# Performance work log

Measured on AMD Instinct MI355X. Metric: run time of the kernel, lower is better.

The kernel has to match this reference:

```python
import jax, jax.numpy as jnp
import numpy as np

N, F, F_, H = 8192, 512, 64, 8
NEG = -1e10

def setup_inputs() -> dict:
    key = jax.random.key(0)
    k1, k2, k3, k4 = jax.random.split(key, 4)
    X = jax.random.normal(k1, (N, F), dtype=jnp.float32)
    A = jax.random.randint(k2, (N, N), 0, 2).astype(jnp.float32)  # dense 0/1 adjacency
    kernels = jax.random.normal(k3, (H, F, F_), dtype=jnp.float32) * 0.05
    attn_kernels = jax.random.normal(k4, (H, 2 * F_), dtype=jnp.float32) * 0.05
    return {"X": X, "A": A, "kernels": kernels, "attn_kernels": attn_kernels}

def reference(X, A, kernels, attn_kernels):
    # Per-head linear transform: [H, N, F_]
    WX = jnp.einsum('nf,hfo->hno', X, kernels)
    a1 = attn_kernels[:, :F_]   # [H, F_] acts on source (row) node
    a2 = attn_kernels[:, F_:]   # [H, F_] acts on target (col) node
    # score[h,i,j] = a1_h . WX[h,i] + a2_h . WX[h,j]  (outer sum, no N^2*2F_ tensor)
    s1 = jnp.einsum('hno,ho->hn', WX, a1)  # [H, N]
    s2 = jnp.einsum('hno,ho->hn', WX, a2)  # [H, N]
    scores = s1[:, :, None] + s2[:, None, :]  # [H, N, N]
    # adjacency mask: A==0 -> -1e10 (note: original has no LeakyReLU)
    masked = jnp.where(A[None, :, :] == 0.0, scores + NEG, scores)
    attn = jax.nn.softmax(masked, axis=-1)  # [H, N, N]
    # dropout is identity at inference (Keras Dropout without training=True)
    feats = jnp.einsum('hnm,hmo->hno', attn, WX)  # [H, N, F_]
    feats = jax.nn.relu(feats)  # concat reduction applies activation per head
    out = jnp.transpose(feats, (1, 0, 2)).reshape(N, H * F_)  # concat heads
    return out
```

## Files before the change

kernel.cpp:

```cpp
#include <hip/hip_runtime.h>
#include <cstdint>

#define NN 8192
#define FF 512
#define FO 64
#define NH 8
#define LDYE 520
#define YPART (8192 * 520)
#define SPLITK 3


typedef __attribute__((ext_vector_type(8))) __bf16 bf16x8;
typedef __attribute__((ext_vector_type(4))) float f32x4;

__device__ __forceinline__ unsigned short f2bf(float f) {
    unsigned int u = __float_as_uint(f);
    u += 0x7fffu + ((u >> 16) & 1u);
    return (unsigned short)(u >> 16);
}

__device__ __forceinline__ void gload16(const void* g, void* l) {
    __builtin_amdgcn_global_load_lds(
        (const __attribute__((address_space(1))) unsigned int*)g,
        (__attribute__((address_space(3))) unsigned int*)l,
        16, 0, 0);
}

__global__ __launch_bounds__(256) void k_convA8(const float* __restrict__ A,
                                                unsigned char* __restrict__ Ab) {
    const int b = blockIdx.x, t = threadIdx.x;
    const int rt = b >> 8;
    const int k16 = ((b & 255) << 1) | (t & 1);
    const int row = t >> 1;
    const uint4* src = (const uint4*)(A + (((size_t)(rt * 128 + row)) << 13) + k16 * 16);
    uint4 f0 = src[0], f1 = src[1], f2 = src[2], f3 = src[3];
#define PK8(v) (((v.x >> 22) & 0x38u) | (((v.y >> 22) & 0x38u) << 8) | \
                (((v.z >> 22) & 0x38u) << 16) | (((v.w >> 22) & 0x38u) << 24))
    uint4 o = {PK8(f0), PK8(f1), PK8(f2), PK8(f3)};
#undef PK8
    size_t G = (((size_t)(rt * 512 + k16)) << 7) + row;
    *(uint4*)(Ab + (G << 4)) = o;
}

__global__ __launch_bounds__(256) void k_prep(const float* __restrict__ X,
                                              const float* __restrict__ Kw,
                                              unsigned short* __restrict__ Xb,
                                              unsigned short* __restrict__ Ktb) {
    const int b = blockIdx.x;
    const int t = threadIdx.x;
    if (b < 2048) {
        size_t base = ((size_t)b * 256 + t) * 8;
        float4 a = *(const float4*)(X + base);
        float4 c = *(const float4*)(X + base + 4);
        ushort4 o0, o1;
        o0.x = f2bf(a.x); o0.y = f2bf(a.y); o0.z = f2bf(a.z); o0.w = f2bf(a.w);
        o1.x = f2bf(c.x); o1.y = f2bf(c.y); o1.z = f2bf(c.z); o1.w = f2bf(c.w);
        *(ushort4*)(Xb + base) = o0;
        *(ushort4*)(Xb + base + 4) = o1;
    } else {
        int h = b - 2048;
        for (int e = t; e < FF * FO; e += 256) {
            int o = e >> 9, f = e & 511;
            Ktb[(size_t)h * FF * FO + e] = f2bf(Kw[(size_t)h * FF * FO + (size_t)f * FO + o]);
        }
    }
}

union WxSmem {
    struct { unsigned short Xs[4096]; unsigned short Ks[2048]; } s;
    unsigned char Vs[64][144];
};

__global__ __launch_bounds__(256) void k_wx(const unsigned short* __restrict__ Xb,
                                            const unsigned short* __restrict__ Ktb,
                                            const float* __restrict__ Aw,
                                            unsigned char* __restrict__ Vt) {
    __shared__ WxSmem sm;
    const int t = threadIdx.x;
    const int n0 = blockIdx.x * 128;
    const int h = blockIdx.y;
    const int lane = t & 63, w = t >> 6;
    const int quad = lane >> 4, l15 = lane & 15;

    const unsigned short* xS0 = Xb + (size_t)(n0 + (t & 127)) * FF + (t >> 7) * 8;
    const unsigned short* xS1 = Xb + (size_t)(n0 + ((t + 256) & 127)) * FF + ((t + 256) >> 7) * 8;
    unsigned short* xD0 = sm.s.Xs + t * 8;
    unsigned short* xD1 = sm.s.Xs + (t + 256) * 8;
    const unsigned short* kS = Ktb + (size_t)h * FF * FO + (size_t)(t & 63) * FF + (t >> 6) * 8;
    unsigned short* kD = sm.s.Ks + t * 8;

    const bf16x8* aF[2];
    const bf16x8* bF[4];
    for (int i = 0; i < 2; ++i)
        aF[i] = (const bf16x8*)(sm.s.Xs + (size_t)(quad * 128 + w * 32 + i * 16 + l15) * 8);
    for (int j = 0; j < 4; ++j)
        bF[j] = (const bf16x8*)(sm.s.Ks + (size_t)(quad * 64 + j * 16 + l15) * 8);

    f32x4 acc[2][4] = {};
    for (int f0 = 0; f0 < FF; f0 += 32) {
        gload16(xS0 + f0, xD0);
        gload16(xS1 + f0, xD1);
        gload16(kS + f0, kD);
        __syncthreads();
        bf16x8 av[2], bv[4];
        for (int i = 0; i < 2; ++i) av[i] = aF[i][0];
        for (int j = 0; j < 4; ++j) bv[j] = bF[j][0];
        for (int i = 0; i < 2; ++i)
            for (int j = 0; j < 4; ++j)
                acc[i][j] = __builtin_amdgcn_mfma_f32_16x16x32_bf16(av[i], bv[j], acc[i][j], 0, 0, 0);
        __syncthreads();
    }

    float a2v[4];
    for (int j = 0; j < 4; ++j) a2v[j] = Aw[h * 128 + 64 + j * 16 + l15];
    float ex[2][4];
    for (int i = 0; i < 2; ++i)
        for (int r = 0; r < 4; ++r) {
            float p = acc[i][0][r] * a2v[0] + acc[i][1][r] * a2v[1]
                    + acc[i][2][r] * a2v[2] + acc[i][3][r] * a2v[3];
            p += __shfl_xor(p, 1);
            p += __shfl_xor(p, 2);
            p += __shfl_xor(p, 4);
            p += __shfl_xor(p, 8);
            ex[i][r] = __expf(p);
        }

    for (int i = 0; i < 2; ++i)
        for (int j = 0; j < 4; ++j) {
            int rowb = w * 32 + i * 16 + quad * 4;
            int col = j * 16 + l15;
            unsigned u = __builtin_amdgcn_cvt_pk_fp8_f32(
                ex[i][0] * acc[i][j][0], ex[i][1] * acc[i][j][1], 0, false);
            u = __builtin_amdgcn_cvt_pk_fp8_f32(
                ex[i][2] * acc[i][j][2], ex[i][3] * acc[i][j][3], (int)u, true);
            *(unsigned*)&sm.Vs[col][rowb] = u;
        }
    __syncthreads();
    for (int j2 = 0; j2 < 2; ++j2) {
        int vid = t + j2 * 256;
        int o = vid >> 3, k16o = vid & 7;
        size_t H = (size_t)((n0 >> 4) + k16o) * 640 + h * 64 + o;
        *(uint4*)(Vt + (H << 4)) = *(const uint4*)&sm.Vs[o][k16o * 16];
    }
    if (l15 == 0) {
        for (int i = 0; i < 2; ++i)
            for (int r = 0; r < 4; ++r) {
                int row = w * 32 + i * 16 + quad * 4 + r;
                unsigned u = __builtin_amdgcn_cvt_pk_fp8_f32(ex[i][r], ex[i][r], 0, false);
                size_t H = (size_t)((n0 >> 4) + (row >> 4)) * 640 + 512 + h;
                Vt[(H << 4) + (row & 15)] = (unsigned char)(u & 0xff);
            }
    }
}

__global__ __launch_bounds__(256) void k_gemm(const unsigned char* __restrict__ Ab,
                                              const unsigned char* __restrict__ Vt,
                                              float* __restrict__ Y) {
    __shared__ unsigned char As[8192];
    __shared__ unsigned char Bs[10240];
    const int t = threadIdx.x;
    const int id = blockIdx.x;
    const int xcd = id & 7;
    const int u = id >> 3;
    const int ct = u & 3;
    const int rp = ((u >> 2) << 3) | xcd;
    const int rt = rp & 63;
    const int part = rp >> 6;
    const int ks0 = (part * 128) / SPLITK;
    const int ks1 = ((part + 1) * 128) / SPLITK;

    const unsigned char* aS0 = Ab + ((size_t)rt << 20) + (size_t)t * 16;
    const unsigned char* aS1 = aS0 + 4096;
    unsigned char* aD0 = As + t * 16;
    unsigned char* aD1 = aD0 + 4096;
    const int g1 = t + 256, g2 = t + 512;
    const unsigned char* bS0 = Vt + (size_t)((t / 160) * 10240 + (ct * 160 + t % 160) * 16);
    const unsigned char* bS1 = Vt + (size_t)((g1 / 160) * 10240 + (ct * 160 + g1 % 160) * 16);
    const unsigned char* bS2 = Vt + (size_t)((g2 / 160) * 10240 + (ct * 160 + g2 % 160) * 16);
    unsigned char* bD0 = Bs + t * 16;
    unsigned char* bD1 = Bs + g1 * 16;
    unsigned char* bD2 = Bs + g2 * 16;

    const int lane = t & 63;
    const int w = t >> 6;
    const int wm = w >> 1, wn = w & 1;
    const int quad = lane >> 4, l15 = lane & 15;

    int aOff[4], bOff[5];
    for (int i = 0; i < 4; ++i)
        aOff[i] = (quad >> 1) * 2048 + (quad & 1) * 8 + (wm * 64 + i * 16 + l15) * 16;
    for (int j = 0; j < 5; ++j)
        bOff[j] = (quad >> 1) * 2560 + (quad & 1) * 8 + (wn * 80 + j * 16 + l15) * 16;

    f32x4 acc[4][5] = {};

    for (int ks = ks0; ks < ks1; ++ks) {
        const size_t koA = (size_t)ks << 13;
        const size_t koB = (size_t)ks * 40960;
        gload16(aS0 + koA, aD0);
        gload16(aS1 + koA, aD1);
        gload16(bS0 + koB, bD0);
        gload16(bS1 + koB, bD1);
        if (t < 128) gload16(bS2 + koB, bD2);
        __syncthreads();
#pragma unroll
        for (int h2 = 0; h2 < 2; ++h2) {
            long long av[4], bv[5];
            for (int i = 0; i < 4; ++i)
                av[i] = *(const long long*)(As + aOff[i] + h2 * 4096);
            for (int j = 0; j < 5; ++j)
                bv[j] = *(const long long*)(Bs + bOff[j] + h2 * 5120);
            for (int i = 0; i < 4; ++i)
                for (int j = 0; j < 5; ++j)
                    acc[i][j] = __builtin_amdgcn_mfma_f32_16x16x32_fp8_fp8(av[i], bv[j], acc[i][j], 0, 0, 0);
        }
        __syncthreads();
    }

    float* Yp = Y + (size_t)part * YPART;
    for (int i = 0; i < 4; ++i) {
        int row = rt * 128 + wm * 64 + i * 16 + quad * 4;
        for (int j = 0; j < 5; ++j) {
            int col = ct * 160 + wn * 80 + j * 16 + l15;
            if (col < 520) {
                for (int r = 0; r < 4; ++r)
                    Yp[(size_t)(row + r) * LDYE + col] = acc[i][j][r];
            }
        }
    }
}

__global__ __launch_bounds__(256) void k_epi(const float* __restrict__ Y,
                                             float* __restrict__ out) {
    int idx = blockIdx.x * 256 + threadIdx.x;
    int n = idx >> 7;
    int c = (idx & 127) * 4;
    int h = c >> 6;
    float4 u = {0.f, 0.f, 0.f, 0.f};
    float den = 0.f;
    const float* yp = Y + (size_t)n * LDYE;
#pragma unroll
    for (int p = 0; p < SPLITK; ++p) {
        float4 v = *(const float4*)(yp + c);
        u.x += v.x; u.y += v.y; u.z += v.z; u.w += v.w;
        den += yp[512 + h];
        yp += (size_t)YPART;
    }
    float inv = 1.0f / den;
    float4 o;
    o.x = fmaxf(u.x * inv, 0.f);
    o.y = fmaxf(u.y * inv, 0.f);
    o.z = fmaxf(u.z * inv, 0.f);
    o.w = fmaxf(u.w * inv, 0.f);
    *(float4*)(out + (size_t)n * 512 + c) = o;
}

extern "C" void kernel_launch(void* const* d_in, const int* in_sizes, int n_in,
                              void* d_out, int out_size, void* d_ws, size_t ws_size,
                              hipStream_t stream) {
    const float* X  = (const float*)d_in[0];
    const float* A  = (const float*)d_in[1];
    const float* Kw = (const float*)d_in[2];
    const float* Aw = (const float*)d_in[3];
    float* out = (float*)d_out;
    char* ws = (char*)d_ws;
    unsigned char* Ab = (unsigned char*)ws;
    unsigned char* Vt = (unsigned char*)(ws + (size_t)67108864);
    float* Yb = (float*)(ws + (size_t)67108864 + (size_t)5242880);
    unsigned short* Xb = (unsigned short*)Yb;
    unsigned short* Ktb = Xb + (size_t)NN * FF;

    k_convA8<<<dim3(16384), dim3(256), 0, stream>>>(A, Ab);
    k_prep<<<dim3(2056), dim3(256), 0, stream>>>(X, Kw, Xb, Ktb);
    k_wx<<<dim3(64, 8), dim3(256), 0, stream>>>(Xb, Ktb, Aw, Vt);
    k_gemm<<<dim3(768), dim3(256), 0, stream>>>(Ab, Vt, Yb);
    k_epi<<<dim3(4096), dim3(256), 0, stream>>>(Yb, out);
}
```

Before: 511.9 us.

## Double-buffer LDS tiles in fp8 GEMM and linearize A conversion stores

The GEMM main loop now uses two LDS buffers, so the global-to-LDS loads for the next k-step are issued before the MFMA work on the current tile, with one barrier per iteration instead of two. This is meant to hide global load latency behind matrix math. It doubles LDS use per block, which may reduce occupancy. The A-to-fp8 conversion kernel is also reindexed so each thread writes consecutive 16-byte chunks, making the stores fully linear, though the reads become strided across rows.

```diff
diff --git a/kernel.cpp b/kernel.cpp
--- a/kernel.cpp
+++ b/kernel.cpp
@@ -28,18 +28,17 @@
 
 __global__ __launch_bounds__(256) void k_convA8(const float* __restrict__ A,
                                                 unsigned char* __restrict__ Ab) {
-    const int b = blockIdx.x, t = threadIdx.x;
-    const int rt = b >> 8;
-    const int k16 = ((b & 255) << 1) | (t & 1);
-    const int row = t >> 1;
-    const uint4* src = (const uint4*)(A + (((size_t)(rt * 128 + row)) << 13) + k16 * 16);
+    const size_t gid = (size_t)blockIdx.x * 256 + threadIdx.x;
+    const int row127 = (int)(gid & 127);
+    const int k16 = (int)((gid >> 7) & 511);
+    const int rt = (int)(gid >> 16);
+    const uint4* src = (const uint4*)(A + (((size_t)(rt * 128 + row127)) << 13) + k16 * 16);
     uint4 f0 = src[0], f1 = src[1], f2 = src[2], f3 = src[3];
 #define PK8(v) (((v.x >> 22) & 0x38u) | (((v.y >> 22) & 0x38u) << 8) | \
                 (((v.z >> 22) & 0x38u) << 16) | (((v.w >> 22) & 0x38u) << 24))
     uint4 o = {PK8(f0), PK8(f1), PK8(f2), PK8(f3)};
 #undef PK8
-    size_t G = (((size_t)(rt * 512 + k16)) << 7) + row;
-    *(uint4*)(Ab + (G << 4)) = o;
+    *(uint4*)(Ab + (gid << 4)) = o;
 }
 
 __global__ __launch_bounds__(256) void k_prep(const float* __restrict__ X,
@@ -156,8 +155,8 @@
 __global__ __launch_bounds__(256) void k_gemm(const unsigned char* __restrict__ Ab,
                                               const unsigned char* __restrict__ Vt,
                                               float* __restrict__ Y) {
-    __shared__ unsigned char As[8192];
-    __shared__ unsigned char Bs[10240];
+    __shared__ unsigned char As0[8192], As1[8192];
+    __shared__ unsigned char Bs0[10240], Bs1[10240];
     const int t = threadIdx.x;
     const int id = blockIdx.x;
     const int xcd = id & 7;
@@ -171,15 +170,10 @@
 
     const unsigned char* aS0 = Ab + ((size_t)rt << 20) + (size_t)t * 16;
     const unsigned char* aS1 = aS0 + 4096;
-    unsigned char* aD0 = As + t * 16;
-    unsigned char* aD1 = aD0 + 4096;
     const int g1 = t + 256, g2 = t + 512;
     const unsigned char* bS0 = Vt + (size_t)((t / 160) * 10240 + (ct * 160 + t % 160) * 16);
     const unsigned char* bS1 = Vt + (size_t)((g1 / 160) * 10240 + (ct * 160 + g1 % 160) * 16);
     const unsigned char* bS2 = Vt + (size_t)((g2 / 160) * 10240 + (ct * 160 + g2 % 160) * 16);
-    unsigned char* bD0 = Bs + t * 16;
-    unsigned char* bD1 = Bs + g1 * 16;
-    unsigned char* bD2 = Bs + g2 * 16;
 
     const int lane = t & 63;
     const int w = t >> 6;
@@ -194,28 +188,49 @@
 
     f32x4 acc[4][5] = {};
 
+#define STAGE(ks, AD, BD)                                                      \
+    do {                                                                       \
+        const size_t koA = (size_t)(ks) << 13;                                 \
+        const size_t koB = (size_t)(ks) * 40960;                               \
+        gload16(aS0 + koA, (AD) + t * 16);                                     \
+        gload16(aS1 + koA, (AD) + 4096 + t * 16);                              \
+        gload16(bS0 + koB, (BD) + t * 16);                                     \
+        gload16(bS1 + koB, (BD) + g1 * 16);                                    \
+        if (t < 128) gload16(bS2 + koB, (BD) + g2 * 16);                       \
+    } while (0)
+
+#define MFMA_TILE(AS, BS)                                                      \
+    do {                                                                       \
+        _Pragma("unroll")                                                      \
+        for (int h2 = 0; h2 < 2; ++h2) {                                       \
+            long long av[4], bv[5];                                            \
+            for (int i = 0; i < 4; ++i)                                        \
+                av[i] = *(const long long*)((AS) + aOff[i] + h2 * 4096);       \
+            for (int j = 0; j < 5; ++j)                                        \
+                bv[j] = *(const long long*)((BS) + bOff[j] + h2 * 5120);       \
+            for (int i = 0; i < 4; ++i)                                        \
+                for (int j = 0; j < 5; ++j)                                    \
+                    acc[i][j] = __builtin_amdgcn_mfma_f32_16x16x32_fp8_fp8(    \
+                        av[i], bv[j], acc[i][j], 0, 0, 0);                     \
+        }                                                                      \
+    } while (0)
+
+    STAGE(ks0, As0, Bs0);
+    __syncthreads();
+    int p = 0;
     for (int ks = ks0; ks < ks1; ++ks) {
-        const size_t koA = (size_t)ks << 13;
-        const size_t koB = (size_t)ks * 40960;
-        gload16(aS0 + koA, aD0);
-        gload16(aS1 + koA, aD1);
-        gload16(bS0 + koB, bD0);
-        gload16(bS1 + koB, bD1);
-        if (t < 128) gload16(bS2 + koB, bD2);
+        if (p == 0) {
+            if (ks + 1 < ks1) STAGE(ks + 1, As1, Bs1);
+            MFMA_TILE(As0, Bs0);
+        } else {
+            if (ks + 1 < ks1) STAGE(ks + 1, As0, Bs0);
+            MFMA_TILE(As1, Bs1);
+        }
         __syncthreads();
-#pragma unroll
-        for (int h2 = 0; h2 < 2; ++h2) {
-            long long av[4], bv[5];
-            for (int i = 0; i < 4; ++i)
-                av[i] = *(const long long*)(As + aOff[i] + h2 * 4096);
-            for (int j = 0; j < 5; ++j)
-                bv[j] = *(const long long*)(Bs + bOff[j] + h2 * 5120);
-            for (int i = 0; i < 4; ++i)
-                for (int j = 0; j < 5; ++j)
-                    acc[i][j] = __builtin_amdgcn_mfma_f32_16x16x32_fp8_fp8(av[i], bv[j], acc[i][j], 0, 0, 0);
-        }
-        __syncthreads();
-    }
+        p ^= 1;
+    }
+#undef STAGE
+#undef MFMA_TILE
 
     float* Yp = Y + (size_t)part * YPART;
     for (int i = 0; i < 4; ++i) {
```

Result: slower. 561.7 us (+9.7%).

## Load GEMM fragments directly from global memory with register double-buffering

Applied to the files above, without the earlier changes.

Changes the fp8 layouts of the adjacency matrix and the V matrix so each lane's MFMA operand is 16 contiguous bytes in global memory. The GEMM then drops its LDS staging and barriers, and instead prefetches the next k-step's fragments into registers while computing the current one. The conversion and WX kernels write the new interleaved layout, with the exponent column staged through shared memory. This removes LDS traffic and block-level synchronisation, but each wave now loads operands from global or L2 with no sharing across waves, which raises global traffic and register pressure.

```diff
diff --git a/kernel.cpp b/kernel.cpp
--- a/kernel.cpp
+++ b/kernel.cpp
@@ -12,6 +12,7 @@
 
 typedef __attribute__((ext_vector_type(8))) __bf16 bf16x8;
 typedef __attribute__((ext_vector_type(4))) float f32x4;
+typedef __attribute__((ext_vector_type(2))) long long llx2;
 
 __device__ __forceinline__ unsigned short f2bf(float f) {
     unsigned int u = __float_as_uint(f);
@@ -28,18 +29,22 @@
 
 __global__ __launch_bounds__(256) void k_convA8(const float* __restrict__ A,
                                                 unsigned char* __restrict__ Ab) {
-    const int b = blockIdx.x, t = threadIdx.x;
-    const int rt = b >> 8;
-    const int k16 = ((b & 255) << 1) | (t & 1);
-    const int row = t >> 1;
-    const uint4* src = (const uint4*)(A + (((size_t)(rt * 128 + row)) << 13) + k16 * 16);
-    uint4 f0 = src[0], f1 = src[1], f2 = src[2], f3 = src[3];
+    const size_t gid = (size_t)blockIdx.x * 256 + threadIdx.x;
+    const int row = (int)(gid & 127);
+    const int q   = (int)((gid >> 7) & 3);
+    const int ks  = (int)((gid >> 9) & 127);
+    const int rt  = (int)(gid >> 16);
+    const float* src = A + (((size_t)(rt * 128 + row)) << 13) + ks * 64 + q * 8;
+    float4 f0 = *(const float4*)(src);
+    float4 f1 = *(const float4*)(src + 4);
+    float4 f2 = *(const float4*)(src + 32);
+    float4 f3 = *(const float4*)(src + 36);
 #define PK8(v) (((v.x >> 22) & 0x38u) | (((v.y >> 22) & 0x38u) << 8) | \
                 (((v.z >> 22) & 0x38u) << 16) | (((v.w >> 22) & 0x38u) << 24))
-    uint4 o = {PK8(f0), PK8(f1), PK8(f2), PK8(f3)};
+    uint4 fi0 = *(uint4*)&f0, fi1 = *(uint4*)&f1, fi2 = *(uint4*)&f2, fi3 = *(uint4*)&f3;
+    uint4 o = {PK8(fi0), PK8(fi1), PK8(fi2), PK8(fi3)};
 #undef PK8
-    size_t G = (((size_t)(rt * 512 + k16)) << 7) + row;
-    *(uint4*)(Ab + (G << 4)) = o;
+    *(uint4*)(Ab + (gid << 4)) = o;
 }
 
 __global__ __launch_bounds__(256) void k_prep(const float* __restrict__ X,
@@ -68,7 +73,7 @@
 
 union WxSmem {
     struct { unsigned short Xs[4096]; unsigned short Ks[2048]; } s;
-    unsigned char Vs[64][144];
+    struct { unsigned char Vs[64][144]; unsigned char Es[128]; } r;
 };
 
 __global__ __launch_bounds__(256) void k_wx(const unsigned short* __restrict__ Xb,
@@ -133,31 +138,38 @@
                 ex[i][0] * acc[i][j][0], ex[i][1] * acc[i][j][1], 0, false);
             u = __builtin_amdgcn_cvt_pk_fp8_f32(
                 ex[i][2] * acc[i][j][2], ex[i][3] * acc[i][j][3], (int)u, true);
-            *(unsigned*)&sm.Vs[col][rowb] = u;
-        }
-    __syncthreads();
-    for (int j2 = 0; j2 < 2; ++j2) {
-        int vid = t + j2 * 256;
-        int o = vid >> 3, k16o = vid & 7;
-        size_t H = (size_t)((n0 >> 4) + k16o) * 640 + h * 64 + o;
-        *(uint4*)(Vt + (H << 4)) = *(const uint4*)&sm.Vs[o][k16o * 16];
-    }
+            *(unsigned*)&sm.r.Vs[col][rowb] = u;
+        }
     if (l15 == 0) {
         for (int i = 0; i < 2; ++i)
             for (int r = 0; r < 4; ++r) {
                 int row = w * 32 + i * 16 + quad * 4 + r;
                 unsigned u = __builtin_amdgcn_cvt_pk_fp8_f32(ex[i][r], ex[i][r], 0, false);
-                size_t H = (size_t)((n0 >> 4) + (row >> 4)) * 640 + 512 + h;
-                Vt[(H << 4) + (row & 15)] = (unsigned char)(u & 0xff);
+                sm.r.Es[row] = (unsigned char)(u & 0xff);
             }
+    }
+    __syncthreads();
+    for (int j2 = 0; j2 < 2; ++j2) {
+        int vid = t + j2 * 256;
+        int o = vid & 63, q = (vid >> 6) & 3, ksl = vid >> 8;
+        const unsigned char* src = &sm.r.Vs[o][ksl * 64 + q * 8];
+        uint2 lo = *(const uint2*)src;
+        uint2 hi = *(const uint2*)(src + 32);
+        uint4 g = {lo.x, lo.y, hi.x, hi.y};
+        *(uint4*)(Vt + (size_t)((n0 >> 6) + ksl) * 40960 + q * 10240 + (h * 64 + o) * 16) = g;
+    }
+    if (t < 8) {
+        int ksl = t >> 2, q = t & 3;
+        uint2 lo = *(const uint2*)&sm.r.Es[ksl * 64 + q * 8];
+        uint2 hi = *(const uint2*)&sm.r.Es[ksl * 64 + 32 + q * 8];
+        uint4 g = {lo.x, lo.y, hi.x, hi.y};
+        *(uint4*)(Vt + (size_t)((n0 >> 6) + ksl) * 40960 + q * 10240 + (512 + h) * 16) = g;
     }
 }
 
 __global__ __launch_bounds__(256) void k_gemm(const unsigned char* __restrict__ Ab,
                                               const unsigned char* __restrict__ Vt,
                                               float* __restrict__ Y) {
-    __shared__ unsigned char As[8192];
-    __shared__ unsigned char Bs[10240];
     const int t = threadIdx.x;
     const int id = blockIdx.x;
     const int xcd = id & 7;
@@ -169,52 +181,40 @@
     const int ks0 = (part * 128) / SPLITK;
     const int ks1 = ((part + 1) * 128) / SPLITK;
 
-    const unsigned char* aS0 = Ab + ((size_t)rt << 20) + (size_t)t * 16;
-    const unsigned char* aS1 = aS0 + 4096;
-    unsigned char* aD0 = As + t * 16;
-    unsigned char* aD1 = aD0 + 4096;
-    const int g1 = t + 256, g2 = t + 512;
-    const unsigned char* bS0 = Vt + (size_t)((t / 160) * 10240 + (ct * 160 + t % 160) * 16);
-    const unsigned char* bS1 = Vt + (size_t)((g1 / 160) * 10240 + (ct * 160 + g1 % 160) * 16);
-    const unsigned char* bS2 = Vt + (size_t)((g2 / 160) * 10240 + (ct * 160 + g2 % 160) * 16);
-    unsigned char* bD0 = Bs + t * 16;
-    unsigned char* bD1 = Bs + g1 * 16;
-    unsigned char* bD2 = Bs + g2 * 16;
-
     const int lane = t & 63;
     const int w = t >> 6;
     const int wm = w >> 1, wn = w & 1;
     const int quad = lane >> 4, l15 = lane & 15;
 
-    int aOff[4], bOff[5];
-    for (int i = 0; i < 4; ++i)
-        aOff[i] = (quad >> 1) * 2048 + (quad & 1) * 8 + (wm * 64 + i * 16 + l15) * 16;
-    for (int j = 0; j < 5; ++j)
-        bOff[j] = (quad >> 1) * 2560 + (quad & 1) * 8 + (wn * 80 + j * 16 + l15) * 16;
+    const unsigned char* aP = Ab + ((size_t)rt << 20) + quad * 2048 + (wm * 64 + l15) * 16;
+    const unsigned char* bP = Vt + quad * 10240 + (ct * 160 + wn * 80 + l15) * 16;
 
     f32x4 acc[4][5] = {};
+    llx2 a_cur[4], b_cur[5];
+    {
+        const unsigned char* ap = aP + (size_t)ks0 * 8192;
+        const unsigned char* bp = bP + (size_t)ks0 * 40960;
+        for (int i = 0; i < 4; ++i) a_cur[i] = *(const llx2*)(ap + i * 256);
+        for (int j = 0; j < 5; ++j) b_cur[j] = *(const llx2*)(bp + j * 256);
+    }
 
     for (int ks = ks0; ks < ks1; ++ks) {
-        const size_t koA = (size_t)ks << 13;
-        const size_t koB = (size_t)ks * 40960;
-        gload16(aS0 + koA, aD0);
-        gload16(aS1 + koA, aD1);
-        gload16(bS0 + koB, bD0);
-        gload16(bS1 + koB, bD1);
-        if (t < 128) gload16(bS2 + koB, bD2);
-        __syncthreads();
-#pragma unroll
-        for (int h2 = 0; h2 < 2; ++h2) {
-            long long av[4], bv[5];
-            for (int i = 0; i < 4; ++i)
-                av[i] = *(const long long*)(As + aOff[i] + h2 * 4096);
+        const int ksn = (ks + 1 < ks1) ? ks + 1 : ks;
+        const unsigned char* ap = aP + (size_t)ksn * 8192;
+        const unsigned char* bp = bP + (size_t)ksn * 40960;
+        llx2 a_nxt[4], b_nxt[5];
+        for (int i = 0; i < 4; ++i) a_nxt[i] = *(const llx2*)(ap + i * 256);
+        for (int j = 0; j < 5; ++j) b_nxt[j] = *(const llx2*)(bp + j * 256);
+        for (int i = 0; i < 4; ++i)
             for (int j = 0; j < 5; ++j)
-                bv[j] = *(const long long*)(Bs + bOff[j] + h2 * 5120);
-            for (int i = 0; i < 4; ++i)
-                for (int j = 0; j < 5; ++j)
-                    acc[i][j] = __builtin_amdgcn_mfma_f32_16x16x32_fp8_fp8(av[i], bv[j], acc[i][j], 0, 0, 0);
-        }
-        __syncthreads();
+                acc[i][j] = __builtin_amdgcn_mfma_f32_16x16x32_fp8_fp8(
+                    a_cur[i].x, b_cur[j].x, acc[i][j], 0, 0, 0);
+        for (int i = 0; i < 4; ++i)
+            for (int j = 0; j < 5; ++j)
+                acc[i][j] = __builtin_amdgcn_mfma_f32_16x16x32_fp8_fp8(
+                    a_cur[i].y, b_cur[j].y, acc[i][j], 0, 0, 0);
+        for (int i = 0; i < 4; ++i) a_cur[i] = a_nxt[i];
+        for (int j = 0; j < 5; ++j) b_cur[j] = b_nxt[j];
     }
 
     float* Yp = Y + (size_t)part * YPART;
```

Measured after the change: 539.9 us. 1.05x slower.
